# Kernel optimization log

Measured on AMD Instinct MI355X. Metric: run time of the kernel, lower is better.

Reference implementation:

```python
import jax, jax.numpy as jnp
import numpy as np

N_HEADS = 16


def setup_inputs() -> dict:
    key = jax.random.key(0)
    ks = jax.random.split(key, 5)
    B, S, D = 2, 2048, 1024
    scale = 1.0 / np.sqrt(D)
    return {
        "x": jax.random.normal(ks[0], (B, S, D), dtype=jnp.float32),
        "w_in": jax.random.normal(ks[1], (3 * D, D), dtype=jnp.float32) * scale,
        "b_in": jax.random.normal(ks[2], (3 * D,), dtype=jnp.float32) * 0.01,
        "w_out": jax.random.normal(ks[3], (D, D), dtype=jnp.float32) * scale,
        "b_out": jax.random.normal(ks[4], (D,), dtype=jnp.float32) * 0.01,
        "mask": 1,
    }


def reference(x, w_in, b_in, w_out, b_out, mask):
    b, s, d = x.shape
    h = N_HEADS
    dh = d // h
    # fused QKV projection (torch Linear: x @ W^T + b)
    qkv = jnp.einsum("bsd,ed->bse", x, w_in) + b_in  # [b, s, 3d]
    q, k, v = jnp.split(qkv, 3, axis=-1)
    # [b, s, d] -> [b, h, s, dh]
    q = q.reshape(b, s, h, dh).transpose(0, 2, 1, 3)
    k = k.reshape(b, s, h, dh).transpose(0, 2, 1, 3)
    v = v.reshape(b, s, h, dh).transpose(0, 2, 1, 3)
    att = jnp.einsum("bhqd,bhkd->bhqk", q, k)
    if mask:
        causal = jnp.triu(jnp.ones((s, s), dtype=bool), k=1)
        att = jnp.where(causal, -jnp.inf, att)
    att = att / jnp.sqrt(jnp.asarray(dh, att.dtype))
    att = jax.nn.softmax(att, axis=-1)
    out = jnp.einsum("bhqk,bhkd->bhqd", att, v)  # [b, h, s, dh]
    out = out.transpose(0, 2, 1, 3).reshape(b, s, d)
    return jnp.einsum("bsd,ed->bse", out, w_out) + b_out
```

## Files before the change

### kernel.cpp

```cpp
#include <hip/hip_runtime.h>
#include <hip/hip_bf16.h>
#include <cmath>

typedef __hip_bfloat16 bf16;
typedef short v8s __attribute__((ext_vector_type(8)));
typedef short v4s __attribute__((ext_vector_type(4)));
typedef float v4f __attribute__((ext_vector_type(4)));
typedef float v16f __attribute__((ext_vector_type(16)));
typedef unsigned v4u __attribute__((ext_vector_type(4)));

#define AS1(p) ((__attribute__((address_space(1))) void*)(p))
#define AS3(p) ((__attribute__((address_space(3))) void*)(p))

__device__ __forceinline__ v4f mfma_bf16(v8s a, v8s b, v4f c) {
    return __builtin_amdgcn_mfma_f32_16x16x32_bf16(a, b, c, 0, 0, 0);
}
__device__ __forceinline__ v16f mfma32(v8s a, v8s b, v16f c) {
    return __builtin_amdgcn_mfma_f32_32x32x16_bf16(a, b, c, 0, 0, 0);
}

__device__ __forceinline__ short bf16_bits(float f) {
    return __builtin_bit_cast(short, __float2bfloat16(f));
}

__device__ __forceinline__ v8s pack4(unsigned a, unsigned b, unsigned c, unsigned d) {
    v4u u = {a, b, c, d};
    return __builtin_bit_cast(v8s, u);
}

__global__ __launch_bounds__(256)
void cvt_all(const float* __restrict__ x, const float* __restrict__ w_in,
             const float* __restrict__ w_out, bf16* __restrict__ xb,
             bf16* __restrict__ wib, bf16* __restrict__ wob)
{
    const int i = blockIdx.x * 256 + threadIdx.x;
    const float* src; bf16* dst; int j;
    if (i < 1048576)      { src = x;     dst = xb;  j = i; }
    else if (i < 1835008) { src = w_in;  dst = wib; j = i - 1048576; }
    else                  { src = w_out; dst = wob; j = i - 1835008; }
    const float4 v = ((const float4*)src)[j];
    v4s p;
    p.x = bf16_bits(v.x); p.y = bf16_bits(v.y);
    p.z = bf16_bits(v.z); p.w = bf16_bits(v.w);
    ((v4s*)dst)[j] = p;
}

template<int NF>
__global__ __launch_bounds__(256)
void gemm_bt(const bf16* __restrict__ A, const bf16* __restrict__ Bt,
             const float* __restrict__ bias, bf16* __restrict__ C,
             float* __restrict__ Cf, int N, int K, int lda)
{
    constexpr int BN = NF * 32;
    __shared__ __align__(16) bf16 As[2][128 * 32];
    __shared__ __align__(16) bf16 Bs[2][BN * 32];

    const int t    = threadIdx.x;
    const int lane = t & 63;
    const int wave = t >> 6;
    const int l16  = lane & 15;
    const int quad = lane >> 4;
    const int m0   = blockIdx.y * 128;
    const int n0   = blockIdx.x * BN;
    const int wm   = (wave >> 1) * 64;
    const int wn   = (wave & 1) * (NF * 16);

    const v4f zf = {0.f, 0.f, 0.f, 0.f};
    v4f acc[4][NF];
#pragma unroll
    for (int i = 0; i < 4; ++i)
#pragma unroll
        for (int j = 0; j < NF; ++j) acc[i][j] = zf;

    const int sr = t >> 2;
    const int g  = ((t & 3) ^ ((sr >> 1) & 3)) * 8;
    const bf16* gA = A  + (size_t)(m0 + sr) * lda + g;
    const bf16* gB = Bt + (size_t)(n0 + sr) * K + g;

    auto stage = [&](int kt, int buf) {
        const int k0 = kt * 32;
        char* lA = (char*)&As[buf][0] + t * 16;
        char* lB = (char*)&Bs[buf][0] + t * 16;
        __builtin_amdgcn_global_load_lds(AS1(gA + k0),                    AS3(lA),        16, 0, 0);
        __builtin_amdgcn_global_load_lds(AS1(gA + (size_t)64 * lda + k0), AS3(lA + 4096), 16, 0, 0);
        __builtin_amdgcn_global_load_lds(AS1(gB + k0),                    AS3(lB),        16, 0, 0);
        if (NF == 4)
            __builtin_amdgcn_global_load_lds(AS1(gB + (size_t)64 * K + k0), AS3(lB + 4096), 16, 0, 0);
    };

    stage(0, 0);
    const int KT = K >> 5;
    const int xs = ((l16 >> 1) & 3) * 8;
    for (int kt = 0; kt < KT; ++kt) {
        const int buf = kt & 1;
        __syncthreads();
        if (kt + 1 < KT) stage(kt + 1, buf ^ 1);

        v8s af[4], bfr[NF];
#pragma unroll
        for (int mi = 0; mi < 4; ++mi)
            af[mi] = *(const v8s*)(&As[buf][0] + (wm + mi * 16 + l16) * 32
                                   + ((quad * 8) ^ xs));
#pragma unroll
        for (int ni = 0; ni < NF; ++ni)
            bfr[ni] = *(const v8s*)(&Bs[buf][0] + (wn + ni * 16 + l16) * 32
                                    + ((quad * 8) ^ xs));
#pragma unroll
        for (int mi = 0; mi < 4; ++mi)
#pragma unroll
            for (int ni = 0; ni < NF; ++ni)
                acc[mi][ni] = mfma_bf16(af[mi], bfr[ni], acc[mi][ni]);
    }

#pragma unroll
    for (int ni = 0; ni < NF; ++ni) {
        const int col = n0 + wn + ni * 16 + l16;
        const float bv = bias[col];
#pragma unroll
        for (int mi = 0; mi < 4; ++mi) {
#pragma unroll
            for (int r = 0; r < 4; ++r) {
                const int row = m0 + wm + mi * 16 + quad * 4 + r;
                const float fv = acc[mi][ni][r] + bv;
                if (Cf) Cf[(size_t)row * N + col] = fv;
                else    C [(size_t)row * N + col] = __float2bfloat16(fv);
            }
        }
    }
}

__global__ __launch_bounds__(256)
void vtrans(const bf16* __restrict__ qkv, bf16* __restrict__ Vt)
{
    __shared__ short Ts[64][72];
    const int t  = threadIdx.x;
    const int st = blockIdx.x;
    const int bh = blockIdx.y;
    const int b = bh >> 4, h = bh & 15;
    const int s0 = st * 64;
    {
        const int i = t >> 2, j0 = (t & 3) * 16;
        const bf16* src = qkv + (size_t)(b * 2048 + s0 + i) * 3072 + 2048 + h * 64 + j0;
        const v8s a0 = *(const v8s*)(src);
        const v8s a1 = *(const v8s*)(src + 8);
        *(v8s*)&Ts[i][j0]     = a0;
        *(v8s*)&Ts[i][j0 + 8] = a1;
    }
    __syncthreads();
    {
        const int d = t >> 2, seg = (t & 3) * 16;
        v8s o0, o1;
#pragma unroll
        for (int m = 0; m < 8; ++m) { o0[m] = Ts[seg + m][d]; o1[m] = Ts[seg + 8 + m][d]; }
        bf16* dst = Vt + (size_t)(bh * 64 + d) * 2048 + s0 + seg;
        *(v8s*)dst       = o0;
        *(v8s*)(dst + 8) = o1;
    }
}

#define M_STATIC 14.0f

__device__ __forceinline__ void softpack(v16f s, int kg0, int qg, bool mask, int hi,
                                         float& lsum, v8s& paE, v8s& paO)
{
    float p[16];
#pragma unroll
    for (int r = 0; r < 16; ++r) {
        float pv = __expf(fmaf(s[r], 0.125f, -M_STATIC));
        if (mask) {
            const int kg = kg0 + (r & 3) + 8 * (r >> 2) + 4 * hi;
            if (kg > qg) pv = 0.f;
        }
        lsum += pv;
        p[r] = pv;
    }
    unsigned P0[4], P1[4];
#pragma unroll
    for (int m = 0; m < 4; ++m) {
        asm("v_cvt_pk_bf16_f32 %0, %1, %2" : "=v"(P0[m]) : "v"(p[4 * m]),     "v"(p[4 * m + 1]));
        asm("v_cvt_pk_bf16_f32 %0, %1, %2" : "=v"(P1[m]) : "v"(p[4 * m + 2]), "v"(p[4 * m + 3]));
    }
    auto sA = __builtin_amdgcn_permlane32_swap(P0[0], P0[1], false, false);
    auto sB = __builtin_amdgcn_permlane32_swap(P1[0], P1[1], false, false);
    auto sC = __builtin_amdgcn_permlane32_swap(P0[2], P0[3], false, false);
    auto sD = __builtin_amdgcn_permlane32_swap(P1[2], P1[3], false, false);
    paE = pack4(sA[0], sB[0], sA[1], sB[1]);
    paO = pack4(sC[0], sD[0], sC[1], sD[1]);
}

__global__ __launch_bounds__(256, 4)
void attn(bf16* __restrict__ qkv, const bf16* __restrict__ Vt)
{
    __shared__ __align__(16) bf16 Ks[2][64 * 64];
    __shared__ __align__(16) bf16 Vs[2][64 * 64];

    const int t    = threadIdx.x;
    const int lane = t & 63;
    const int w    = t >> 6;
    const int wq   = w >> 1;
    const int wk   = w & 1;
    const int l31  = lane & 31;
    const int hi   = lane >> 5;
    const int id   = blockIdx.x;
    const int bh   = id & 31;
    const int qb   = 31 - (id >> 5);
    const int b = bh >> 4, h = bh & 15;
    const int T = qb + 1;
    const int rowq  = qb * 64 + wq * 32;
    const int qg    = rowq + l31;
    const int ndiag = 2 * qb + wq;

    v8s qf[4];
    {
        const bf16* Qb = qkv + (size_t)(b * 2048 + qg) * 3072 + h * 64 + hi * 8;
#pragma unroll
        for (int c = 0; c < 4; ++c) qf[c] = *(const v8s*)(Qb + c * 16);
    }

    const int sl    = t & 31;
    const int chunk = 2 * ((t >> 6) & 3) + ((t >> 5) & 1);
    const bf16* kbase = qkv + (size_t)(b * 2048 + sl) * 3072 + 1024 + h * 64 + chunk * 8;
    const bf16* vbase = Vt + (size_t)(bh * 64 + sl) * 2048 + chunk * 8;

    auto stage = [&](int tile, int bufi) {
        char* kd = (char*)&Ks[bufi][0] + t * 16;
        char* vd = (char*)&Vs[bufi][0] + t * 16;
        const bf16* ks0 = kbase + (size_t)(tile * 64) * 3072;
        const bf16* vs0 = vbase + tile * 64;
        __builtin_amdgcn_global_load_lds(AS1(ks0),                   AS3(kd),        16, 0, 0);
        __builtin_amdgcn_global_load_lds(AS1(ks0 + (size_t)32*3072), AS3(kd + 4096), 16, 0, 0);
        __builtin_amdgcn_global_load_lds(AS1(vs0),                   AS3(vd),        16, 0, 0);
        __builtin_amdgcn_global_load_lds(AS1(vs0 + (size_t)32*2048), AS3(vd + 4096), 16, 0, 0);
    };

    stage(0, 0);

    v16f o0 = {}, o1 = {};
    float lsum = 0.f;
    const int kfoff = wk * 2048 + lane * 8;
    const int vb0   = wk * 1024 + lane * 8;

    for (int tile = 0; tile < T; ++tile) {
        const int buf = tile & 1;
        __syncthreads();
        if (tile + 1 < T) stage(tile + 1, buf ^ 1);

        const int m_ = 2 * tile + wk;
        if (m_ <= ndiag) {
            const bf16* Kb = &Ks[buf][0];
            const bf16* Vb = &Vs[buf][0];

            v16f s = {};
#pragma unroll
            for (int c = 0; c < 4; ++c)
                s = mfma32(*(const v8s*)(Kb + kfoff + c * 512), qf[c], s);

            v8s paE, paO;
            softpack(s, tile * 64 + 32 * wk, qg, m_ == ndiag, hi, lsum, paE, paO);

            o0 = mfma32(paE, *(const v8s*)(Vb + vb0),            o0);
            o1 = mfma32(paE, *(const v8s*)(Vb + vb0 + 4 * 512),  o1);
            o0 = mfma32(paO, *(const v8s*)(Vb + vb0 + 512),      o0);
            o1 = mfma32(paO, *(const v8s*)(Vb + vb0 + 5 * 512),  o1);
        }
    }

    __syncthreads();
    float* Rp = (float*)&Ks[0][0];
    float* Lp = (float*)&Vs[0][0];
    if (wk) {
        float* R = Rp + wq * 2048 + lane * 32;
#pragma unroll
        for (int j = 0; j < 4; ++j) {
            v4f a = { o0[4*j], o0[4*j+1], o0[4*j+2], o0[4*j+3] };
            ((v4f*)R)[j ^ (lane & 7)] = a;
        }
#pragma unroll
        for (int j = 0; j < 4; ++j) {
            v4f a = { o1[4*j], o1[4*j+1], o1[4*j+2], o1[4*j+3] };
            ((v4f*)R)[(4 + j) ^ (lane & 7)] = a;
        }
        Lp[wq * 64 + lane] = lsum;
    }
    __syncthreads();
    if (!wk) {
        const float* R = Rp + wq * 2048 + lane * 32;
#pragma unroll
        for (int j = 0; j < 4; ++j) {
            v4f a = ((const v4f*)R)[j ^ (lane & 7)];
#pragma unroll
            for (int e = 0; e < 4; ++e) o0[4*j + e] += a[e];
        }
#pragma unroll
        for (int j = 0; j < 4; ++j) {
            v4f a = ((const v4f*)R)[(4 + j) ^ (lane & 7)];
#pragma unroll
            for (int e = 0; e < 4; ++e) o1[4*j + e] += a[e];
        }
        lsum += Lp[wq * 64 + lane];
        const float lt = lsum + __shfl_xor(lsum, 32);

        bf16* dst0 = qkv + (size_t)(b * 2048 + rowq) * 3072 + 2048 + h * 64 + l31;
#pragma unroll
        for (int r = 0; r < 16; ++r) {
            const int q = (r & 3) + 8 * (r >> 2) + 4 * hi;
            const float rs  = fmaxf(__shfl(lt, q), 1e-30f);
            const float inv = 1.0f / rs;
            bf16* dst = dst0 + (size_t)q * 3072;
            dst[0]  = __float2bfloat16(o0[r] * inv);
            dst[32] = __float2bfloat16(o1[r] * inv);
        }
    }
}

extern "C" void kernel_launch(void* const* d_in, const int* in_sizes, int n_in,
                              void* d_out, int out_size, void* d_ws, size_t ws_size,
                              hipStream_t stream)
{
    (void)in_sizes; (void)n_in; (void)out_size; (void)ws_size;
    const float* x     = (const float*)d_in[0];
    const float* w_in  = (const float*)d_in[1];
    const float* b_in  = (const float*)d_in[2];
    const float* w_out = (const float*)d_in[3];
    const float* b_out = (const float*)d_in[4];
    float* out = (float*)d_out;

    bf16* ws     = (bf16*)d_ws;
    bf16* xb     = ws;
    bf16* w_inb  = xb     + (size_t)4096 * 1024;
    bf16* w_outb = w_inb  + (size_t)3072 * 1024;
    bf16* qkv    = w_outb + (size_t)1024 * 1024;
    bf16* vt     = (bf16*)d_out;

    cvt_all<<<8192, 256, 0, stream>>>(x, w_in, w_out, xb, w_inb, w_outb);

    gemm_bt<4><<<dim3(24, 32), dim3(256), 0, stream>>>(xb, w_inb, b_in, qkv, nullptr,
                                                       3072, 1024, 1024);
    vtrans<<<dim3(32, 32), dim3(256), 0, stream>>>(qkv, vt);
    attn<<<1024, 256, 0, stream>>>(qkv, vt);
    gemm_bt<2><<<dim3(16, 32), dim3(256), 0, stream>>>(qkv + 2048, w_outb, b_out, nullptr,
                                                       out, 1024, 1024, 3072);
}
```

Baseline: 196.9 us.

## Fuse V transpose into QKV GEMM epilogue, use 512-thread GEMM, swizzle block order

The QKV GEMM epilogue now writes the V columns directly in transposed layout, which removes the separate vtrans kernel and its extra pass over V. The GEMM moves to 512 threads (8 waves, each owning a 32-row slice), so each thread issues one staging load instead of two. Workgroup IDs are swizzled in both GEMM and attention to change which tiles run together and improve L2 locality. In exchange, each wave has fewer accumulators and less register reuse, and the transposed V stores are narrower 8-byte writes.

Result: faster. 187.3 us (-4.9%).

```diff
diff --git a/kernel.cpp b/kernel.cpp
--- a/kernel.cpp
+++ b/kernel.cpp
@@ -46,10 +46,11 @@
 }
 
 template<int NF>
-__global__ __launch_bounds__(256)
+__global__ __launch_bounds__(512, 4)
 void gemm_bt(const bf16* __restrict__ A, const bf16* __restrict__ Bt,
              const float* __restrict__ bias, bf16* __restrict__ C,
-             float* __restrict__ Cf, int N, int K, int lda)
+             float* __restrict__ Cf, bf16* __restrict__ VtOut,
+             int N, int K, int lda)
 {
     constexpr int BN = NF * 32;
     __shared__ __align__(16) bf16 As[2][128 * 32];
@@ -57,18 +58,23 @@
 
     const int t    = threadIdx.x;
     const int lane = t & 63;
-    const int wave = t >> 6;
+    const int w    = t >> 6;
     const int l16  = lane & 15;
     const int quad = lane >> 4;
-    const int m0   = blockIdx.y * 128;
-    const int n0   = blockIdx.x * BN;
-    const int wm   = (wave >> 1) * 64;
-    const int wn   = (wave & 1) * (NF * 16);
+
+    const int nwg  = gridDim.x * gridDim.y;
+    const int orig = blockIdx.y * gridDim.x + blockIdx.x;
+    const int swz  = (orig & 7) * (nwg >> 3) + (orig >> 3);
+    const int m0   = (swz / gridDim.x) * 128;
+    const int n0   = (swz % gridDim.x) * BN;
+
+    const int wm   = (w & 3) * 32;
+    const int wn   = (w >> 2) * (NF * 16);
 
     const v4f zf = {0.f, 0.f, 0.f, 0.f};
-    v4f acc[4][NF];
-#pragma unroll
-    for (int i = 0; i < 4; ++i)
+    v4f acc[2][NF];
+#pragma unroll
+    for (int i = 0; i < 2; ++i)
 #pragma unroll
         for (int j = 0; j < NF; ++j) acc[i][j] = zf;
 
@@ -79,13 +85,9 @@
 
     auto stage = [&](int kt, int buf) {
         const int k0 = kt * 32;
-        char* lA = (char*)&As[buf][0] + t * 16;
-        char* lB = (char*)&Bs[buf][0] + t * 16;
-        __builtin_amdgcn_global_load_lds(AS1(gA + k0),                    AS3(lA),        16, 0, 0);
-        __builtin_amdgcn_global_load_lds(AS1(gA + (size_t)64 * lda + k0), AS3(lA + 4096), 16, 0, 0);
-        __builtin_amdgcn_global_load_lds(AS1(gB + k0),                    AS3(lB),        16, 0, 0);
-        if (NF == 4)
-            __builtin_amdgcn_global_load_lds(AS1(gB + (size_t)64 * K + k0), AS3(lB + 4096), 16, 0, 0);
+        __builtin_amdgcn_global_load_lds(AS1(gA + k0), AS3((char*)&As[buf][0] + t * 16), 16, 0, 0);
+        if (NF == 4 || t < 256)
+            __builtin_amdgcn_global_load_lds(AS1(gB + k0), AS3((char*)&Bs[buf][0] + t * 16), 16, 0, 0);
     };
 
     stage(0, 0);
@@ -96,9 +98,9 @@
         __syncthreads();
         if (kt + 1 < KT) stage(kt + 1, buf ^ 1);
 
-        v8s af[4], bfr[NF];
-#pragma unroll
-        for (int mi = 0; mi < 4; ++mi)
+        v8s af[2], bfr[NF];
+#pragma unroll
+        for (int mi = 0; mi < 2; ++mi)
             af[mi] = *(const v8s*)(&As[buf][0] + (wm + mi * 16 + l16) * 32
                                    + ((quad * 8) ^ xs));
 #pragma unroll
@@ -106,55 +108,46 @@
             bfr[ni] = *(const v8s*)(&Bs[buf][0] + (wn + ni * 16 + l16) * 32
                                     + ((quad * 8) ^ xs));
 #pragma unroll
-        for (int mi = 0; mi < 4; ++mi)
+        for (int mi = 0; mi < 2; ++mi)
 #pragma unroll
             for (int ni = 0; ni < NF; ++ni)
                 acc[mi][ni] = mfma_bf16(af[mi], bfr[ni], acc[mi][ni]);
     }
 
-#pragma unroll
-    for (int ni = 0; ni < NF; ++ni) {
-        const int col = n0 + wn + ni * 16 + l16;
-        const float bv = bias[col];
-#pragma unroll
-        for (int mi = 0; mi < 4; ++mi) {
-#pragma unroll
-            for (int r = 0; r < 4; ++r) {
-                const int row = m0 + wm + mi * 16 + quad * 4 + r;
-                const float fv = acc[mi][ni][r] + bv;
-                if (Cf) Cf[(size_t)row * N + col] = fv;
-                else    C [(size_t)row * N + col] = __float2bfloat16(fv);
+    if (VtOut != nullptr && n0 >= 2048) {
+        const int bb   = m0 >> 11;
+        const int srow = (m0 & 2047) + wm;
+#pragma unroll
+        for (int ni = 0; ni < NF; ++ni) {
+            const int col = n0 + wn + ni * 16 + l16;
+            const int hd  = col - 2048;
+            const float bv = bias[col];
+            bf16* vdst = VtOut + (size_t)(bb * 1024 + hd) * 2048 + srow;
+#pragma unroll
+            for (int mi = 0; mi < 2; ++mi) {
+                v4s p;
+#pragma unroll
+                for (int r = 0; r < 4; ++r)
+                    p[r] = bf16_bits(acc[mi][ni][r] + bv);
+                *(v4s*)(vdst + mi * 16 + quad * 4) = p;
             }
         }
-    }
-}
-
-__global__ __launch_bounds__(256)
-void vtrans(const bf16* __restrict__ qkv, bf16* __restrict__ Vt)
-{
-    __shared__ short Ts[64][72];
-    const int t  = threadIdx.x;
-    const int st = blockIdx.x;
-    const int bh = blockIdx.y;
-    const int b = bh >> 4, h = bh & 15;
-    const int s0 = st * 64;
-    {
-        const int i = t >> 2, j0 = (t & 3) * 16;
-        const bf16* src = qkv + (size_t)(b * 2048 + s0 + i) * 3072 + 2048 + h * 64 + j0;
-        const v8s a0 = *(const v8s*)(src);
-        const v8s a1 = *(const v8s*)(src + 8);
-        *(v8s*)&Ts[i][j0]     = a0;
-        *(v8s*)&Ts[i][j0 + 8] = a1;
-    }
-    __syncthreads();
-    {
-        const int d = t >> 2, seg = (t & 3) * 16;
-        v8s o0, o1;
-#pragma unroll
-        for (int m = 0; m < 8; ++m) { o0[m] = Ts[seg + m][d]; o1[m] = Ts[seg + 8 + m][d]; }
-        bf16* dst = Vt + (size_t)(bh * 64 + d) * 2048 + s0 + seg;
-        *(v8s*)dst       = o0;
-        *(v8s*)(dst + 8) = o1;
+    } else {
+#pragma unroll
+        for (int ni = 0; ni < NF; ++ni) {
+            const int col = n0 + wn + ni * 16 + l16;
+            const float bv = bias[col];
+#pragma unroll
+            for (int mi = 0; mi < 2; ++mi) {
+#pragma unroll
+                for (int r = 0; r < 4; ++r) {
+                    const int row = m0 + wm + mi * 16 + quad * 4 + r;
+                    const float fv = acc[mi][ni][r] + bv;
+                    if (Cf) Cf[(size_t)row * N + col] = fv;
+                    else    C [(size_t)row * N + col] = __float2bfloat16(fv);
+                }
+            }
+        }
     }
 }
 
@@ -202,8 +195,9 @@
     const int l31  = lane & 31;
     const int hi   = lane >> 5;
     const int id   = blockIdx.x;
-    const int bh   = id & 31;
-    const int qb   = 31 - (id >> 5);
+    const int j    = id >> 3;
+    const int bh   = (id & 7) * 4 + (j & 3);
+    const int qb   = 31 - (j >> 2);
     const int b = bh >> 4, h = bh & 15;
     const int T = qb + 1;
     const int rowq  = qb * 64 + wq * 32;
@@ -271,14 +265,14 @@
     if (wk) {
         float* R = Rp + wq * 2048 + lane * 32;
 #pragma unroll
-        for (int j = 0; j < 4; ++j) {
-            v4f a = { o0[4*j], o0[4*j+1], o0[4*j+2], o0[4*j+3] };
-            ((v4f*)R)[j ^ (lane & 7)] = a;
-        }
-#pragma unroll
-        for (int j = 0; j < 4; ++j) {
-            v4f a = { o1[4*j], o1[4*j+1], o1[4*j+2], o1[4*j+3] };
-            ((v4f*)R)[(4 + j) ^ (lane & 7)] = a;
+        for (int j2 = 0; j2 < 4; ++j2) {
+            v4f a = { o0[4*j2], o0[4*j2+1], o0[4*j2+2], o0[4*j2+3] };
+            ((v4f*)R)[j2 ^ (lane & 7)] = a;
+        }
+#pragma unroll
+        for (int j2 = 0; j2 < 4; ++j2) {
+            v4f a = { o1[4*j2], o1[4*j2+1], o1[4*j2+2], o1[4*j2+3] };
+            ((v4f*)R)[(4 + j2) ^ (lane & 7)] = a;
         }
         Lp[wq * 64 + lane] = lsum;
     }
@@ -286,16 +280,16 @@
     if (!wk) {
         const float* R = Rp + wq * 2048 + lane * 32;
 #pragma unroll
-        for (int j = 0; j < 4; ++j) {
-            v4f a = ((const v4f*)R)[j ^ (lane & 7)];
-#pragma unroll
-            for (int e = 0; e < 4; ++e) o0[4*j + e] += a[e];
-        }
-#pragma unroll
-        for (int j = 0; j < 4; ++j) {
-            v4f a = ((const v4f*)R)[(4 + j) ^ (lane & 7)];
-#pragma unroll
-            for (int e = 0; e < 4; ++e) o1[4*j + e] += a[e];
+        for (int j2 = 0; j2 < 4; ++j2) {
+            v4f a = ((const v4f*)R)[j2 ^ (lane & 7)];
+#pragma unroll
+            for (int e = 0; e < 4; ++e) o0[4*j2 + e] += a[e];
+        }
+#pragma unroll
+        for (int j2 = 0; j2 < 4; ++j2) {
+            v4f a = ((const v4f*)R)[(4 + j2) ^ (lane & 7)];
+#pragma unroll
+            for (int e = 0; e < 4; ++e) o1[4*j2 + e] += a[e];
         }
         lsum += Lp[wq * 64 + lane];
         const float lt = lsum + __shfl_xor(lsum, 32);
@@ -334,10 +328,9 @@
 
     cvt_all<<<8192, 256, 0, stream>>>(x, w_in, w_out, xb, w_inb, w_outb);
 
-    gemm_bt<4><<<dim3(24, 32), dim3(256), 0, stream>>>(xb, w_inb, b_in, qkv, nullptr,
-                                                       3072, 1024, 1024);
-    vtrans<<<dim3(32, 32), dim3(256), 0, stream>>>(qkv, vt);
+    gemm_bt<4><<<dim3(24, 32), dim3(512), 0, stream>>>(xb, w_inb, b_in, qkv, nullptr,
+                                                       vt, 3072, 1024, 1024);
     attn<<<1024, 256, 0, stream>>>(qkv, vt);
-    gemm_bt<2><<<dim3(16, 32), dim3(256), 0, stream>>>(qkv + 2048, w_outb, b_out, nullptr,
-                                                       out, 1024, 1024, 3072);
-}
+    gemm_bt<2><<<dim3(16, 32), dim3(512), 0, stream>>>(qkv + 2048, w_outb, b_out, nullptr,
+                                                       out, nullptr, 1024, 1024, 3072);
+}
```
